# Optimization experiments

Measured on AMD Instinct MI355X. Metric: run time of the kernel, lower is better.

Reference implementation:

```python
import jax, jax.numpy as jnp
import numpy as np

# Module hyperparameters (from init_kwargs)
B, C, E, T = 8, 128, 128, 128          # batch, in_channels, embedding(freq), time
O, G, KW, KS = 256, 4, 9, 1            # out_channels, groups, kernel_width, kernel_stride
D = C // G                              # kernel depth per group = 32
N = O // G                              # filters per group = 64
AH, AS = 2, 2                           # activate_height, activate_stride
NEG_SLOPE = 0.01                        # nn.LeakyReLU default


def setup_inputs() -> dict:
    key = jax.random.key(0)
    kx, kw = jax.random.split(key)
    x = jax.random.normal(kx, (B, C, E, T), dtype=jnp.float32)
    # xavier_uniform over (O, D, E, KW): fan_in = D*E*KW, fan_out = O*E*KW
    fan_in, fan_out = D * E * KW, O * E * KW
    limit = float(np.sqrt(6.0 / (fan_in + fan_out)))
    weight = jax.random.uniform(kw, (O, D, E, KW), dtype=jnp.float32,
                                minval=-limit, maxval=limit)
    return {"x": x, "weight": weight}


def reference(x, weight):
    b, c, e, t = x.shape
    # --- symmetric-ish zero pad along time so unfold yields exactly t windows ---
    pad = (t - 1) * KS - t + KW
    xp = jnp.pad(x, ((0, 0), (0, 0), (0, 0), (pad // 2, (pad + 1) // 2)))
    # --- unfold: windows of size KW at stride KS -> (b, c, e, t, KW) ---
    idx = jnp.arange(t)[:, None] * KS + jnp.arange(KW)[None, :]  # (t, KW)
    xu = xp[..., idx]                                            # (b, c, e, t, KW)
    # --- grouped linear-conv: instead of materializing (b,t,g,n,d,e,KW), contract d,KW ---
    xu = xu.reshape(b, G, D, e, t, KW)                 # (b, g, d, e, t, w)
    wr = weight.reshape(G, N, D, e, KW)                # (g, n, d, e, w)
    # z[b,g,n,e,t] = sum_{d,w} xu * wr  (the all-ones conv sums over d and full width w)
    z = jnp.einsum('bgdetw,gndew->bgnet', xu, wr).reshape(b, O, e, t)
    # --- all-ones conv height pooling: kernel AH, stride AS over e (valid) ---
    f_out = (e - AH) // AS + 1
    cs = jnp.cumsum(z, axis=2)
    cs = jnp.concatenate([jnp.zeros_like(cs[:, :, :1]), cs], axis=2)  # prefix sums
    pos = jnp.arange(f_out) * AS
    pooled = cs[:, :, pos + AH, :] - cs[:, :, pos, :]   # (b, O, f_out, t)
    # --- LeakyReLU ---
    y = jnp.where(pooled >= 0, pooled, NEG_SLOPE * pooled)
    return y  # (b, o, f_out, t), matching 'b o f t'
```

## Files before the change

### kernel.cpp

```cpp
#include <hip/hip_runtime.h>
#include <cstddef>

typedef __attribute__((ext_vector_type(8))) short short8v;
typedef __attribute__((ext_vector_type(4))) short short4v;
typedef __attribute__((ext_vector_type(4))) float f32x4;

__device__ __forceinline__ unsigned short f2bf(float f) {
    unsigned u = __float_as_uint(f);
    u = (u + 0x7FFFu + ((u >> 16) & 1u)) >> 16;
    return (unsigned short)u;
}

__global__ __launch_bounds__(256) void prep_w(const float* __restrict__ w,
                                              unsigned short* __restrict__ wb)
{
    const int g  = blockIdx.x >> 6;
    const int f  = blockIdx.x & 63;
    const int e0 = 2 * f;
    const int tid = threadIdx.x;
    __shared__ unsigned short ls[64 * 580];

    #pragma unroll 4
    for (int i = 0; i < 72; ++i) {
        int fl  = tid + i * 256;
        int od  = fl / 9;
        int f2i = fl - od * 9;
        int o_l = od >> 5;
        int d   = od & 31;
        const float2 v = *reinterpret_cast<const float2*>(
            &w[(size_t)((g * 64 + o_l) * 32 + d) * 1152 + e0 * 9 + f2i * 2]);
        ushort2 hh; hh.x = f2bf(v.x); hh.y = f2bf(v.y);
        *reinterpret_cast<ushort2*>(&ls[o_l * 580 + d * 18 + f2i * 2]) = hh;
    }
    __syncthreads();

    unsigned short* wo = wb + (size_t)(g * 64 + f) * 36864;
    #pragma unroll 2
    for (int i = 0; i < 18; ++i) {
        int oc   = tid + i * 256;
        int ks   = oc >> 8;
        int nt   = (oc >> 6) & 3;
        int lane = oc & 63;
        int li = lane & 15, hi = lane >> 4;
        int ec = (ks >= 9) ? 1 : 0;
        int w9 = ks - 9 * ec;
        int o_l = nt * 16 + li;
        short8v vv;
        #pragma unroll
        for (int j = 0; j < 8; ++j)
            vv[j] = (short)ls[o_l * 580 + (hi * 8 + j) * 18 + ec * 9 + w9];
        *reinterpret_cast<short8v*>(&wo[(size_t)oc * 8]) = vv;
    }
}

__global__ __launch_bounds__(256, 2) void lconv_mfma(const float* __restrict__ x,
                                                     const unsigned short* __restrict__ wb,
                                                     float* __restrict__ out)
{
    int bid = blockIdx.x;
    int lid = (bid & 7) * 64 + (bid >> 3);
    const int h = lid & 1;
    const int f = (lid >> 1) & 63;
    const int g = lid >> 7;
    const int e0 = 2 * f;

    const int tid  = threadIdx.x;
    const int lane = tid & 63;
    const int wv   = tid >> 6;
    const int bl   = wv & 1;
    const int th   = wv >> 1;
    const int li   = lane & 15;
    const int hi   = lane >> 4;
    const int t    = tid & 127;
    const int z    = tid >> 7;

    __shared__ __align__(16) unsigned short xs[2 * 136 * 40];
    __shared__ __align__(16) unsigned short As[18432];

    if (tid < 128) {
        int blz = tid >> 6;
        int r   = (tid >> 3) & 7;
        int dq  = tid & 7;
        int tp  = (r < 4) ? r : (128 + r);
        short4v zz = {0, 0, 0, 0};
        *reinterpret_cast<short4v*>(&xs[(blz * 136 + tp) * 40 + dq * 4]) = zz;
    }

    const unsigned short* wslab = wb + (size_t)(g * 64 + f) * 36864;

    float   xr[32];
    short8v ar[9];

    f32x4 acc[4][4];
    #pragma unroll
    for (int nt = 0; nt < 4; ++nt)
        #pragma unroll
        for (int tt = 0; tt < 4; ++tt)
            acc[nt][tt] = (f32x4){0.f, 0.f, 0.f, 0.f};

    auto issue = [&](int p) {
        const int e  = e0 + (p & 1);
        const int b0 = h * 4 + (p >> 1) * 2 + z;
        const float* xp0 = &x[((size_t)(b0 * 128 + g * 32) * 128 + e) * 128 + t];
        #pragma unroll
        for (int i = 0; i < 8; ++i) {
            const float* xp = xp0 + (size_t)i * 4 * 16384;
            xr[i * 4 + 0] = xp[0];
            xr[i * 4 + 1] = xp[16384];
            xr[i * 4 + 2] = xp[32768];
            xr[i * 4 + 3] = xp[49152];
        }
        const short8v* src = reinterpret_cast<const short8v*>(wslab + (size_t)(p & 1) * 18432);
        #pragma unroll
        for (int i = 0; i < 9; ++i) ar[i] = src[tid + i * 256];
    };

    auto lwrite = [&]() {
        #pragma unroll
        for (int i = 0; i < 8; ++i) {
            short4v hq;
            hq[0] = (short)f2bf(xr[i * 4 + 0]);
            hq[1] = (short)f2bf(xr[i * 4 + 1]);
            hq[2] = (short)f2bf(xr[i * 4 + 2]);
            hq[3] = (short)f2bf(xr[i * 4 + 3]);
            *reinterpret_cast<short4v*>(&xs[(z * 136 + t + 4) * 40 + i * 4]) = hq;
        }
        short8v* dst = reinterpret_cast<short8v*>(As);
        #pragma unroll
        for (int i = 0; i < 9; ++i) dst[tid + i * 256] = ar[i];
    };

    auto compute = [&]() {
        #pragma unroll
        for (int w9 = 0; w9 < 9; ++w9) {
            short8v Af[4], Bf[4];
            #pragma unroll
            for (int nt = 0; nt < 4; ++nt)
                Af[nt] = *reinterpret_cast<const short8v*>(
                    &As[(w9 * 4 + nt) * 512 + lane * 8]);
            #pragma unroll
            for (int tt = 0; tt < 4; ++tt) {
                int tp = th * 64 + tt * 16 + li + w9;
                Bf[tt] = *reinterpret_cast<const short8v*>(
                    &xs[(bl * 136 + tp) * 40 + hi * 8]);
            }
            #pragma unroll
            for (int nt = 0; nt < 4; ++nt)
                #pragma unroll
                for (int tt = 0; tt < 4; ++tt)
                    acc[nt][tt] = __builtin_amdgcn_mfma_f32_16x16x32_bf16(
                        Af[nt], Bf[tt], acc[nt][tt], 0, 0, 0);
        }
    };

    auto store_tile = [&](int tl) {
        const int b = h * 4 + tl * 2 + bl;
        #pragma unroll
        for (int nt = 0; nt < 4; ++nt)
            #pragma unroll
            for (int tt = 0; tt < 4; ++tt)
                #pragma unroll
                for (int j = 0; j < 4; ++j) {
                    float v = acc[nt][tt][j];
                    v = (v >= 0.f) ? v : 0.01f * v;
                    int n  = nt * 16 + hi * 4 + j;
                    int tc = th * 64 + tt * 16 + li;
                    out[(((size_t)(b * 256 + g * 64 + n)) * 64 + f) * 128 + tc] = v;
                }
    };

    issue(0);
    lwrite();
    __syncthreads();

    issue(1);
    compute();
    __syncthreads();
    lwrite();
    __syncthreads();

    issue(2);
    compute();
    store_tile(0);
    #pragma unroll
    for (int nt = 0; nt < 4; ++nt)
        #pragma unroll
        for (int tt = 0; tt < 4; ++tt)
            acc[nt][tt] = (f32x4){0.f, 0.f, 0.f, 0.f};
    __syncthreads();
    lwrite();
    __syncthreads();

    issue(3);
    compute();
    __syncthreads();
    lwrite();
    __syncthreads();

    compute();
    store_tile(1);
}

extern "C" void kernel_launch(void* const* d_in, const int* in_sizes, int n_in,
                              void* d_out, int out_size, void* d_ws, size_t ws_size,
                              hipStream_t stream)
{
    const float* x = (const float*)d_in[0];
    const float* w = (const float*)d_in[1];
    float* out = (float*)d_out;
    unsigned short* wb = (unsigned short*)d_ws;

    hipLaunchKernelGGL(prep_w, dim3(256), dim3(256), 0, stream, w, wb);
    hipLaunchKernelGGL(lconv_mfma, dim3(512), dim3(256), 0, stream, x, wb, out);
}
```

Baseline: 53.40 us.

## Split weight staging into halves, double grid, raise occupancy to three blocks

Weight tiles are re-laid out in prep_w so each e-slice splits into two halves of five and four kernel taps. The main kernel now stages only half a weight slice in LDS at a time, which shrinks shared memory and registers and allows three blocks per CU. Each block now covers one batch pair instead of two, doubling the grid to 1024 blocks. Compute phases are wrapped in s_setprio to favour MFMA issue. The cost is more barriers per block and reloading each weight slice from global memory twice as often.

```diff
diff --git a/kernel.cpp b/kernel.cpp
--- a/kernel.cpp
+++ b/kernel.cpp
@@ -42,26 +42,29 @@
         int nt   = (oc >> 6) & 3;
         int lane = oc & 63;
         int li = lane & 15, hi = lane >> 4;
-        int ec = (ks >= 9) ? 1 : 0;
-        int w9 = ks - 9 * ec;
+        int e  = (ks >= 9) ? 1 : 0;
+        int w9 = ks - 9 * e;
         int o_l = nt * 16 + li;
         short8v vv;
         #pragma unroll
         for (int j = 0; j < 8; ++j)
-            vv[j] = (short)ls[o_l * 580 + (hi * 8 + j) * 18 + ec * 9 + w9];
-        *reinterpret_cast<short8v*>(&wo[(size_t)oc * 8]) = vv;
-    }
-}
-
-__global__ __launch_bounds__(256, 2) void lconv_mfma(const float* __restrict__ x,
+            vv[j] = (short)ls[o_l * 580 + (hi * 8 + j) * 18 + e * 9 + w9];
+        int half = (w9 < 5) ? 0 : 1;
+        int w9l  = w9 - 5 * half;
+        size_t off = (size_t)e * 18432 + half * 10240 + (w9l * 4 + nt) * 512 + lane * 8;
+        *reinterpret_cast<short8v*>(&wo[off]) = vv;
+    }
+}
+
+__global__ __launch_bounds__(256, 3) void lconv_mfma(const float* __restrict__ x,
                                                      const unsigned short* __restrict__ wb,
                                                      float* __restrict__ out)
 {
     int bid = blockIdx.x;
-    int lid = (bid & 7) * 64 + (bid >> 3);
-    const int h = lid & 1;
-    const int f = (lid >> 1) & 63;
-    const int g = lid >> 7;
+    int lid = (bid & 7) * 128 + (bid >> 3);
+    const int bp = lid & 3;
+    const int f  = (lid >> 2) & 63;
+    const int g  = lid >> 8;
     const int e0 = 2 * f;
 
     const int tid  = threadIdx.x;
@@ -75,7 +78,7 @@
     const int z    = tid >> 7;
 
     __shared__ __align__(16) unsigned short xs[2 * 136 * 40];
-    __shared__ __align__(16) unsigned short As[18432];
+    __shared__ __align__(16) unsigned short As[10240];
 
     if (tid < 128) {
         int blz = tid >> 6;
@@ -86,10 +89,10 @@
         *reinterpret_cast<short4v*>(&xs[(blz * 136 + tp) * 40 + dq * 4]) = zz;
     }
 
-    const unsigned short* wslab = wb + (size_t)(g * 64 + f) * 36864;
+    const unsigned short* wA = wb + (size_t)(g * 64 + f) * 36864;
 
     float   xr[32];
-    short8v ar[9];
+    short8v ar[5];
 
     f32x4 acc[4][4];
     #pragma unroll
@@ -98,107 +101,114 @@
         for (int tt = 0; tt < 4; ++tt)
             acc[nt][tt] = (f32x4){0.f, 0.f, 0.f, 0.f};
 
-    auto issue = [&](int p) {
-        const int e  = e0 + (p & 1);
-        const int b0 = h * 4 + (p >> 1) * 2 + z;
+    auto issueX = [&](int ec) {
+        const int e  = e0 + ec;
+        const int b0 = bp * 2 + z;
         const float* xp0 = &x[((size_t)(b0 * 128 + g * 32) * 128 + e) * 128 + t];
         #pragma unroll
-        for (int i = 0; i < 8; ++i) {
-            const float* xp = xp0 + (size_t)i * 4 * 16384;
-            xr[i * 4 + 0] = xp[0];
-            xr[i * 4 + 1] = xp[16384];
-            xr[i * 4 + 2] = xp[32768];
-            xr[i * 4 + 3] = xp[49152];
-        }
-        const short8v* src = reinterpret_cast<const short8v*>(wslab + (size_t)(p & 1) * 18432);
-        #pragma unroll
-        for (int i = 0; i < 9; ++i) ar[i] = src[tid + i * 256];
-    };
-
-    auto lwrite = [&]() {
-        #pragma unroll
-        for (int i = 0; i < 8; ++i) {
+        for (int dq = 0; dq < 8; ++dq) {
+            const float* xp = xp0 + (size_t)dq * 4 * 16384;
+            xr[dq * 4 + 0] = xp[0];
+            xr[dq * 4 + 1] = xp[16384];
+            xr[dq * 4 + 2] = xp[32768];
+            xr[dq * 4 + 3] = xp[49152];
+        }
+    };
+    auto lwriteX = [&]() {
+        #pragma unroll
+        for (int dq = 0; dq < 8; ++dq) {
             short4v hq;
-            hq[0] = (short)f2bf(xr[i * 4 + 0]);
-            hq[1] = (short)f2bf(xr[i * 4 + 1]);
-            hq[2] = (short)f2bf(xr[i * 4 + 2]);
-            hq[3] = (short)f2bf(xr[i * 4 + 3]);
-            *reinterpret_cast<short4v*>(&xs[(z * 136 + t + 4) * 40 + i * 4]) = hq;
-        }
+            hq[0] = (short)f2bf(xr[dq * 4 + 0]);
+            hq[1] = (short)f2bf(xr[dq * 4 + 1]);
+            hq[2] = (short)f2bf(xr[dq * 4 + 2]);
+            hq[3] = (short)f2bf(xr[dq * 4 + 3]);
+            *reinterpret_cast<short4v*>(&xs[(z * 136 + t + 4) * 40 + dq * 4]) = hq;
+        }
+    };
+    auto issueA = [&](int ec, int h) {
+        const short8v* src = reinterpret_cast<const short8v*>(
+            wA + (size_t)ec * 18432 + h * 10240);
+        const int cnt = h ? 4 : 5;
+        #pragma unroll
+        for (int i = 0; i < 5; ++i)
+            if (i < cnt) ar[i] = src[tid + i * 256];
+    };
+    auto lwriteA = [&](int h) {
         short8v* dst = reinterpret_cast<short8v*>(As);
-        #pragma unroll
-        for (int i = 0; i < 9; ++i) dst[tid + i * 256] = ar[i];
-    };
-
-    auto compute = [&]() {
-        #pragma unroll
-        for (int w9 = 0; w9 < 9; ++w9) {
+        const int cnt = h ? 4 : 5;
+        #pragma unroll
+        for (int i = 0; i < 5; ++i)
+            if (i < cnt) dst[tid + i * 256] = ar[i];
+    };
+    auto compute = [&](int h) {
+        const int cnt = h ? 4 : 5;
+        const int wb9 = h ? 5 : 0;
+        #pragma unroll
+        for (int w9l = 0; w9l < 5; ++w9l) {
+            if (w9l >= cnt) break;
             short8v Af[4], Bf[4];
             #pragma unroll
             for (int nt = 0; nt < 4; ++nt)
                 Af[nt] = *reinterpret_cast<const short8v*>(
-                    &As[(w9 * 4 + nt) * 512 + lane * 8]);
+                    &As[(w9l * 4 + nt) * 512 + lane * 8]);
             #pragma unroll
             for (int tt = 0; tt < 4; ++tt) {
-                int tp = th * 64 + tt * 16 + li + w9;
+                int tp = th * 64 + tt * 16 + li + wb9 + w9l;
                 Bf[tt] = *reinterpret_cast<const short8v*>(
                     &xs[(bl * 136 + tp) * 40 + hi * 8]);
             }
+            __builtin_amdgcn_s_setprio(1);
             #pragma unroll
             for (int nt = 0; nt < 4; ++nt)
                 #pragma unroll
                 for (int tt = 0; tt < 4; ++tt)
                     acc[nt][tt] = __builtin_amdgcn_mfma_f32_16x16x32_bf16(
                         Af[nt], Bf[tt], acc[nt][tt], 0, 0, 0);
-        }
-    };
-
-    auto store_tile = [&](int tl) {
-        const int b = h * 4 + tl * 2 + bl;
-        #pragma unroll
-        for (int nt = 0; nt < 4; ++nt)
-            #pragma unroll
-            for (int tt = 0; tt < 4; ++tt)
-                #pragma unroll
-                for (int j = 0; j < 4; ++j) {
-                    float v = acc[nt][tt][j];
-                    v = (v >= 0.f) ? v : 0.01f * v;
-                    int n  = nt * 16 + hi * 4 + j;
-                    int tc = th * 64 + tt * 16 + li;
-                    out[(((size_t)(b * 256 + g * 64 + n)) * 64 + f) * 128 + tc] = v;
-                }
-    };
-
-    issue(0);
-    lwrite();
-    __syncthreads();
-
-    issue(1);
-    compute();
-    __syncthreads();
-    lwrite();
-    __syncthreads();
-
-    issue(2);
-    compute();
-    store_tile(0);
+            __builtin_amdgcn_s_setprio(0);
+        }
+    };
+
+    issueX(0); issueA(0, 0);
+    lwriteX(); lwriteA(0);
+    __syncthreads();
+
+    issueA(0, 1);
+    compute(0);
+    __syncthreads();
+    lwriteA(1);
+    __syncthreads();
+
+    issueX(1);
+    compute(1);
+    __syncthreads();
+    lwriteX();
+    issueA(1, 0);
+    lwriteA(0);
+    __syncthreads();
+
+    issueA(1, 1);
+    compute(0);
+    __syncthreads();
+    lwriteA(1);
+    __syncthreads();
+
+    compute(1);
+
+    const int b = bp * 2 + bl;
     #pragma unroll
-    for (int nt = 0; nt < 4; ++nt)
-        #pragma unroll
-        for (int tt = 0; tt < 4; ++tt)
-            acc[nt][tt] = (f32x4){0.f, 0.f, 0.f, 0.f};
-    __syncthreads();
-    lwrite();
-    __syncthreads();
-
-    issue(3);
-    compute();
-    __syncthreads();
-    lwrite();
-    __syncthreads();
-
-    compute();
-    store_tile(1);
+    for (int nt = 0; nt < 4; ++nt) {
+        #pragma unroll
+        for (int tt = 0; tt < 4; ++tt) {
+            #pragma unroll
+            for (int j = 0; j < 4; ++j) {
+                float v = acc[nt][tt][j];
+                v = (v >= 0.f) ? v : 0.01f * v;
+                int n  = nt * 16 + hi * 4 + j;
+                int tc = th * 64 + tt * 16 + li;
+                out[(((size_t)(b * 256 + g * 64 + n)) * 64 + f) * 128 + tc] = v;
+            }
+        }
+    }
 }
 
 extern "C" void kernel_launch(void* const* d_in, const int* in_sizes, int n_in,
@@ -211,5 +221,5 @@
     unsigned short* wb = (unsigned short*)d_ws;
 
     hipLaunchKernelGGL(prep_w, dim3(256), dim3(256), 0, stream, w, wb);
-    hipLaunchKernelGGL(lconv_mfma, dim3(512), dim3(256), 0, stream, x, wb, out);
-}
+    hipLaunchKernelGGL(lconv_mfma, dim3(1024), dim3(256), 0, stream, x, wb, out);
+}
```

New measurement: 61.64 us. 1.15x slower.
